# Optimization experiments

Measured on AMD Instinct MI355X. Metric: run time of the kernel, lower is better.

Reference implementation:

```python
import jax, jax.numpy as jnp
import numpy as np

D_MODEL = 2048
NUM_HEADS = 32
NUM_GROUPS = 8
HEAD_DIM = D_MODEL // NUM_HEADS  # 64
HPG = NUM_HEADS // NUM_GROUPS    # heads per group = 4
B, S = 2, 2048


def setup_inputs() -> dict:
    key = jax.random.key(0)
    ks = jax.random.split(key, 11)
    sd = 1.0 / np.sqrt(D_MODEL)
    kv_dim = HEAD_DIM * NUM_GROUPS
    return {
        "q": jax.random.normal(ks[0], (B, S, D_MODEL), jnp.float32),
        "k": jax.random.normal(ks[1], (B, S, D_MODEL), jnp.float32),
        "v": jax.random.normal(ks[2], (B, S, D_MODEL), jnp.float32),
        "Wq": jax.random.normal(ks[3], (D_MODEL, D_MODEL), jnp.float32) * sd,
        "bq": jnp.zeros((D_MODEL,), jnp.float32),
        "Wk": jax.random.normal(ks[4], (D_MODEL, kv_dim), jnp.float32) * sd,
        "bk": jnp.zeros((kv_dim,), jnp.float32),
        "Wv": jax.random.normal(ks[5], (D_MODEL, kv_dim), jnp.float32) * sd,
        "bv": jnp.zeros((kv_dim,), jnp.float32),
        "Wo": jax.random.normal(ks[6], (D_MODEL, D_MODEL), jnp.float32) * sd,
        "bo": jnp.zeros((D_MODEL,), jnp.float32),
    }


def reference(q, k, v, Wq, bq, Wk, bk, Wv, bv, Wo, bo):
    b, qlen, _ = q.shape
    kvlen = k.shape[1]
    # projections
    qh = (q @ Wq + bq).reshape(b, qlen, NUM_GROUPS, HPG, HEAD_DIM)   # [b,s,g,h,d]
    kh = (k @ Wk + bk).reshape(b, kvlen, NUM_GROUPS, HEAD_DIM)        # [b,t,g,d]
    vh = (v @ Wv + bv).reshape(b, kvlen, NUM_GROUPS, HEAD_DIM)        # [b,t,g,d]
    scale = 1.0 / np.sqrt(HEAD_DIM).astype(np.float32)
    # grouped attention: each group's heads share the same K/V
    scores = jnp.einsum('bsghd,btgd->bghst', qh, kh) * scale          # [b,g,h,s,t]
    attn = jax.nn.softmax(scores, axis=-1)                            # dropout = identity (eval)
    out = jnp.einsum('bghst,btgd->bsghd', attn, vh)                   # [b,s,g,h,d]
    out = out.reshape(b, qlen, D_MODEL)
    return out @ Wo + bo
```

## Files before the change

kernel.cpp:

```cpp
#include <hip/hip_runtime.h>

typedef unsigned short u16;
typedef unsigned int u32;
typedef __attribute__((ext_vector_type(8))) short bf16x8;
typedef __attribute__((ext_vector_type(4))) float f32x4;
typedef __attribute__((ext_vector_type(16))) float f32x16;

#define DM 2048
#define SQ_SCALE (0.125f * 1.44269504089f)

__device__ __forceinline__ u16 f2bf(float f) {
  union { float f; u32 u; } v; v.f = f;
  u32 r = v.u + 0x7fffu + ((v.u >> 16) & 1u);
  return (u16)(r >> 16);
}
__device__ __forceinline__ u32 pkrn(float lo, float hi) {
  union { float f; u32 u; } a, b; a.f = lo; b.f = hi;
  return ((a.u + 0x8000u) >> 16) | ((b.u + 0x8000u) & 0xffff0000u);
}
__device__ __forceinline__ void gload16(const u16* g, u16* l) {
  __builtin_amdgcn_global_load_lds((const __attribute__((address_space(1))) void*)g,
                                   (__attribute__((address_space(3))) void*)l, 16, 0, 0);
}

__global__ __launch_bounds__(256) void cast3(const float* __restrict__ a0,
                                             const float* __restrict__ a1,
                                             const float* __restrict__ a2,
                                             u16* __restrict__ o0,
                                             u16* __restrict__ o1,
                                             u16* __restrict__ o2) {
  const float* in; u16* out;
  if (blockIdx.z == 0) { in = a0; out = o0; }
  else if (blockIdx.z == 1) { in = a1; out = o1; }
  else { in = a2; out = o2; }
  size_t i = ((size_t)blockIdx.x * 256 + threadIdx.x) * 8;
  float4 f0 = *(const float4*)(in + i);
  float4 f1 = *(const float4*)(in + i + 4);
  uint4 w = {pkrn(f0.x, f0.y), pkrn(f0.z, f0.w), pkrn(f1.x, f1.y), pkrn(f1.z, f1.w)};
  *(uint4*)(out + i) = w;
}

__global__ __launch_bounds__(256) void transpose_cast(const float* __restrict__ in,
                                                      u16* __restrict__ out,
                                                      int K, int N) {
  __shared__ u16 s[64][72];
  int n0 = blockIdx.x * 64, k0 = blockIdx.y * 64;
  int t = threadIdx.x;
  int r = t >> 2;
  int cc = (t & 3) * 16;
  const float* ip = in + (size_t)(k0 + r) * N + n0 + cc;
  u16 tmp[16];
#pragma unroll
  for (int i = 0; i < 16; i += 4) {
    float4 v = *(const float4*)(ip + i);
    tmp[i] = f2bf(v.x); tmp[i + 1] = f2bf(v.y);
    tmp[i + 2] = f2bf(v.z); tmp[i + 3] = f2bf(v.w);
  }
  *(uint4*)&s[r][cc] = *(uint4*)tmp;
  *(uint4*)&s[r][cc + 8] = *(uint4*)(tmp + 8);
  __syncthreads();
#pragma unroll
  for (int i = 0; i < 16; i++) tmp[i] = s[cc + i][r];
  u16* op = out + (size_t)(n0 + r) * K + k0 + cc;
  *(uint4*)op = *(uint4*)tmp;
  *(uint4*)(op + 8) = *(uint4*)(tmp + 8);
}

__global__ __launch_bounds__(256) void transpose_v(const u16* __restrict__ kvb,
                                                   u16* __restrict__ vtb) {
  __shared__ u16 s[64][72];
  int bg = blockIdx.y;
  int t0 = blockIdx.x * 64;
  int t = threadIdx.x;
  int r = t >> 2;
  int cc = (t & 3) * 16;
  const u16* ip = kvb + ((size_t)(bg >> 3) * 2048 + t0 + r) * 1024 + 512 + (bg & 7) * 64 + cc;
  *(uint4*)&s[r][cc] = *(const uint4*)ip;
  *(uint4*)&s[r][cc + 8] = *(const uint4*)(ip + 8);
  __syncthreads();
  u16 tmp[16];
#pragma unroll
  for (int i = 0; i < 16; i++) tmp[i] = s[cc + i][r];
  u16* op = vtb + (size_t)bg * 64 * 2048 + (size_t)r * 2048 + t0 + cc;
  *(uint4*)op = *(uint4*)tmp;
  *(uint4*)(op + 8) = *(uint4*)(tmp + 8);
}

__global__ __launch_bounds__(256) void gemm_proj(const u16* __restrict__ qb,
                                                 const u16* __restrict__ kb,
                                                 const u16* __restrict__ vb,
                                                 const u16* __restrict__ Bt,
                                                 const float* __restrict__ bqp,
                                                 const float* __restrict__ bkp,
                                                 const float* __restrict__ bvp,
                                                 u16* __restrict__ qhb,
                                                 u16* __restrict__ kvb) {
  __shared__ u16 As[128 * 32];
  __shared__ u16 Bs[128 * 32];
  int n0 = blockIdx.x * 128, m0 = blockIdx.y * 128;
  const u16* A; const float* bias; u16* C; int cw, bofs; float esc;
  if (n0 < 2048)      { A = qb; bias = bqp; C = qhb; cw = 2048; bofs = 0;    esc = SQ_SCALE; }
  else if (n0 < 2560) { A = kb; bias = bkp; C = kvb; cw = 1024; bofs = 2048; esc = 1.0f; }
  else                { A = vb; bias = bvp; C = kvb; cw = 1024; bofs = 2560; esc = 1.0f; }
  int ccol0 = (n0 < 2048) ? n0 : (n0 - 2048);

  int tid = threadIdx.x, wave = tid >> 6, lane = tid & 63;
  int lq = lane & 15, quad = lane >> 4;
  int wm = (wave & 1) * 64, wn = (wave >> 1) * 64;

  f32x4 zero = {0.f, 0.f, 0.f, 0.f};
  f32x4 acc[4][4];
#pragma unroll
  for (int i = 0; i < 4; i++)
#pragma unroll
    for (int j = 0; j < 4; j++) acc[i][j] = zero;

  const u16* gA = A + (size_t)(m0 + wave * 16 + (lane >> 2)) * 2048 + (lane & 3) * 8;
  const u16* gB = Bt + (size_t)(n0 + wave * 16 + (lane >> 2)) * 2048 + (lane & 3) * 8;
  u16* lA0 = &As[(wave * 16) * 32];
  u16* lA1 = &As[(64 + wave * 16) * 32];
  u16* lB0 = &Bs[(wave * 16) * 32];
  u16* lB1 = &Bs[(64 + wave * 16) * 32];

  for (int k0 = 0; k0 < 2048; k0 += 32) {
    __syncthreads();
    gload16(gA + k0, lA0);
    gload16(gA + (size_t)64 * 2048 + k0, lA1);
    gload16(gB + k0, lB0);
    gload16(gB + (size_t)64 * 2048 + k0, lB1);
    __syncthreads();
    bf16x8 af[4], bf[4];
#pragma unroll
    for (int i = 0; i < 4; i++) af[i] = *(const bf16x8*)&As[(wm + i * 16 + lq) * 32 + quad * 8];
#pragma unroll
    for (int j = 0; j < 4; j++) bf[j] = *(const bf16x8*)&Bs[(wn + j * 16 + lq) * 32 + quad * 8];
#pragma unroll
    for (int i = 0; i < 4; i++)
#pragma unroll
      for (int j = 0; j < 4; j++)
        acc[i][j] = __builtin_amdgcn_mfma_f32_16x16x32_bf16(af[i], bf[j], acc[i][j], 0, 0, 0);
  }
#pragma unroll
  for (int j = 0; j < 4; j++) {
    int nglob = n0 + wn + j * 16 + lq;
    float bv = bias[nglob - bofs];
    int col = ccol0 + wn + j * 16 + lq;
#pragma unroll
    for (int i = 0; i < 4; i++) {
#pragma unroll
      for (int rg = 0; rg < 4; rg++) {
        int row = m0 + wm + i * 16 + quad * 4 + rg;
        C[(size_t)row * cw + col] = f2bf((acc[i][j][rg] + bv) * esc);
      }
    }
  }
}

__global__ __launch_bounds__(256) void gemm_o(const u16* __restrict__ A,
                                              const u16* __restrict__ Bt,
                                              const float* __restrict__ bias,
                                              float* __restrict__ C) {
  __shared__ u16 As[128 * 32];
  __shared__ u16 Bs[128 * 32];
  int n0 = blockIdx.x * 128, m0 = blockIdx.y * 128;
  int tid = threadIdx.x, wave = tid >> 6, lane = tid & 63;
  int lq = lane & 15, quad = lane >> 4;
  int wm = (wave & 1) * 64, wn = (wave >> 1) * 64;

  f32x4 zero = {0.f, 0.f, 0.f, 0.f};
  f32x4 acc[4][4];
#pragma unroll
  for (int i = 0; i < 4; i++)
#pragma unroll
    for (int j = 0; j < 4; j++) acc[i][j] = zero;

  const u16* gA = A + (size_t)(m0 + wave * 16 + (lane >> 2)) * 2048 + (lane & 3) * 8;
  const u16* gB = Bt + (size_t)(n0 + wave * 16 + (lane >> 2)) * 2048 + (lane & 3) * 8;
  u16* lA0 = &As[(wave * 16) * 32];
  u16* lA1 = &As[(64 + wave * 16) * 32];
  u16* lB0 = &Bs[(wave * 16) * 32];
  u16* lB1 = &Bs[(64 + wave * 16) * 32];

  for (int k0 = 0; k0 < 2048; k0 += 32) {
    __syncthreads();
    gload16(gA + k0, lA0);
    gload16(gA + (size_t)64 * 2048 + k0, lA1);
    gload16(gB + k0, lB0);
    gload16(gB + (size_t)64 * 2048 + k0, lB1);
    __syncthreads();
    bf16x8 af[4], bf[4];
#pragma unroll
    for (int i = 0; i < 4; i++) af[i] = *(const bf16x8*)&As[(wm + i * 16 + lq) * 32 + quad * 8];
#pragma unroll
    for (int j = 0; j < 4; j++) bf[j] = *(const bf16x8*)&Bs[(wn + j * 16 + lq) * 32 + quad * 8];
#pragma unroll
    for (int i = 0; i < 4; i++)
#pragma unroll
      for (int j = 0; j < 4; j++)
        acc[i][j] = __builtin_amdgcn_mfma_f32_16x16x32_bf16(af[i], bf[j], acc[i][j], 0, 0, 0);
  }
#pragma unroll
  for (int j = 0; j < 4; j++) {
    int col = n0 + wn + j * 16 + lq;
    float bv = bias[col];
#pragma unroll
    for (int i = 0; i < 4; i++) {
#pragma unroll
      for (int rg = 0; rg < 4; rg++) {
        int row = m0 + wm + i * 16 + quad * 4 + rg;
        C[(size_t)row * 2048 + col] = acc[i][j][rg] + bv;
      }
    }
  }
}

__global__ __launch_bounds__(256) void attn2(const u16* __restrict__ qh,
                                             const u16* __restrict__ kvb,
                                             const u16* __restrict__ vtb,
                                             u16* __restrict__ out) {
  __shared__ u16 Ks[32][72];
  __shared__ u16 Vs[64][40];
  __shared__ float Ls[4][2][32];
  int flat = blockIdx.x + (blockIdx.y << 3);
  int w = ((flat & 7) << 6) + (flat >> 3);
  int head = w >> 3;
  int b = head >> 5, g = (head >> 2) & 7, h = head & 3;
  int tid = threadIdx.x, wave = tid >> 6, lane = tid & 63;
  int lh = lane & 31, hi = lane >> 5;
  const int qoff = (g * 4 + h) * 64;
  const int koff = g * 64;
  int sBase = (w & 7) * 256 + wave * 64;

  bf16x8 qf[2][4];
#pragma unroll
  for (int sb = 0; sb < 2; sb++)
#pragma unroll
    for (int st = 0; st < 4; st++)
      qf[sb][st] = *(const bf16x8*)(qh + (size_t)(b * 2048 + sBase + sb * 32 + lh) * DM +
                                    qoff + st * 16 + hi * 8);

  f32x16 o_acc[2][2];
#pragma unroll
  for (int sb = 0; sb < 2; sb++)
#pragma unroll
    for (int db = 0; db < 2; db++)
#pragma unroll
      for (int r = 0; r < 16; r++) o_acc[sb][db][r] = 0.f;
  float l_acc[2] = {0.f, 0.f};

  int sr = tid >> 3, sc = (tid & 7) * 8;
  int vd = tid >> 2, vc = (tid & 3) * 8;
  const u16* kbase = kvb + (size_t)b * 2048 * 1024 + koff;
  const u16* vbase = vtb + (size_t)(head >> 2) * 64 * 2048 + (size_t)vd * 2048;

  uint4 kreg = *(const uint4*)(kbase + (size_t)sr * 1024 + sc);
  uint4 vreg = *(const uint4*)(vbase + vc);

  for (int t0 = 0; t0 < 2048; t0 += 32) {
    __syncthreads();
    *(uint4*)&Ks[sr][sc] = kreg;
    *(uint4*)&Vs[vd][vc] = vreg;
    __syncthreads();
    int tn = (t0 + 32 < 2048) ? t0 + 32 : 0;
    kreg = *(const uint4*)(kbase + (size_t)(tn + sr) * 1024 + sc);
    vreg = *(const uint4*)(vbase + tn + vc);

    bf16x8 kf[4], vf[2][2];
#pragma unroll
    for (int st = 0; st < 4; st++) kf[st] = *(const bf16x8*)&Ks[lh][st * 16 + hi * 8];
#pragma unroll
    for (int T = 0; T < 2; T++)
#pragma unroll
      for (int db = 0; db < 2; db++)
        vf[T][db] = *(const bf16x8*)&Vs[db * 32 + lh][T * 16 + hi * 8];

#pragma unroll
    for (int sb = 0; sb < 2; sb++) {
      f32x16 st_acc;
#pragma unroll
      for (int r = 0; r < 16; r++) st_acc[r] = 0.f;
      __builtin_amdgcn_s_setprio(1);
#pragma unroll
      for (int st = 0; st < 4; st++)
        st_acc = __builtin_amdgcn_mfma_f32_32x32x16_bf16(kf[st], qf[sb][st], st_acc, 0, 0, 0);
      __builtin_amdgcn_s_setprio(0);
      float pr[16];
#pragma unroll
      for (int r = 0; r < 16; r++) pr[r] = __builtin_amdgcn_exp2f(st_acc[r]);
      float s0 = ((pr[0] + pr[1]) + (pr[2] + pr[3])) + ((pr[4] + pr[5]) + (pr[6] + pr[7]));
      float s1 = ((pr[8] + pr[9]) + (pr[10] + pr[11])) + ((pr[12] + pr[13]) + (pr[14] + pr[15]));
      l_acc[sb] += s0 + s1;
      u32 pk[8];
#pragma unroll
      for (int a = 0; a < 4; a++) {
        pk[2 * a] = pkrn(pr[4 * a], pr[4 * a + 1]);
        pk[2 * a + 1] = pkrn(pr[4 * a + 2], pr[4 * a + 3]);
      }
#pragma unroll
      for (int T = 0; T < 2; T++) {
        u32 E0 = hi ? pk[4 * T] : pk[4 * T + 2];
        u32 E1 = hi ? pk[4 * T + 1] : pk[4 * T + 3];
        u32 X0 = __shfl_xor(E0, 32);
        u32 X1 = __shfl_xor(E1, 32);
        union { u32 u[4]; bf16x8 v; } af;
        af.u[0] = hi ? X0 : pk[4 * T];
        af.u[1] = hi ? X1 : pk[4 * T + 1];
        af.u[2] = hi ? pk[4 * T + 2] : X0;
        af.u[3] = hi ? pk[4 * T + 3] : X1;
        __builtin_amdgcn_s_setprio(1);
#pragma unroll
        for (int db = 0; db < 2; db++)
          o_acc[sb][db] = __builtin_amdgcn_mfma_f32_32x32x16_bf16(af.v, vf[T][db], o_acc[sb][db], 0, 0, 0);
        __builtin_amdgcn_s_setprio(0);
      }
    }
  }

#pragma unroll
  for (int sb = 0; sb < 2; sb++) {
    float lt = l_acc[sb] + __shfl_xor(l_acc[sb], 32);
    Ls[wave][sb][lh] = 1.0f / lt;
  }
  __builtin_amdgcn_wave_barrier();
#pragma unroll
  for (int sb = 0; sb < 2; sb++) {
    f32x4 inv[4];
#pragma unroll
    for (int a = 0; a < 4; a++) inv[a] = *(const f32x4*)&Ls[wave][sb][8 * a + 4 * hi];
#pragma unroll
    for (int db = 0; db < 2; db++) {
#pragma unroll
      for (int r = 0; r < 16; r++) {
        int srow = (r & 3) + 8 * (r >> 2) + 4 * hi;
        size_t o = (size_t)(b * 2048 + sBase + sb * 32 + srow) * DM + qoff + db * 32 + lh;
        out[o] = f2bf(o_acc[sb][db][r] * inv[r >> 2][r & 3]);
      }
    }
  }
}

extern "C" void kernel_launch(void* const* d_in, const int* in_sizes, int n_in,
                              void* d_out, int out_size, void* d_ws, size_t ws_size,
                              hipStream_t stream) {
  const float* q  = (const float*)d_in[0];
  const float* k  = (const float*)d_in[1];
  const float* v  = (const float*)d_in[2];
  const float* Wq = (const float*)d_in[3];
  const float* bq = (const float*)d_in[4];
  const float* Wk = (const float*)d_in[5];
  const float* bk = (const float*)d_in[6];
  const float* Wv = (const float*)d_in[7];
  const float* bv = (const float*)d_in[8];
  const float* Wo = (const float*)d_in[9];
  const float* bo = (const float*)d_in[10];

  u16* p = (u16*)d_ws;
  u16* WqkvT = p; p += (size_t)3072 * 2048;
  u16* WoT   = p; p += (size_t)2048 * 2048;
  u16* qb    = p; p += (size_t)4096 * 2048;
  u16* kb    = p; p += (size_t)4096 * 2048;
  u16* vb    = p; p += (size_t)4096 * 2048;
  u16* qhb   = p; p += (size_t)4096 * 2048;
  u16* kvb   = p; p += (size_t)4096 * 1024;
  u16* vtb   = p; p += (size_t)16 * 64 * 2048;
  u16* att   = qb;

  cast3<<<dim3(4096, 1, 3), 256, 0, stream>>>(q, k, v, qb, kb, vb);

  transpose_cast<<<dim3(32, 32), 256, 0, stream>>>(Wq, WqkvT, 2048, 2048);
  transpose_cast<<<dim3(8, 32), 256, 0, stream>>>(Wk, WqkvT + (size_t)2048 * 2048, 2048, 512);
  transpose_cast<<<dim3(8, 32), 256, 0, stream>>>(Wv, WqkvT + (size_t)2560 * 2048, 2048, 512);
  transpose_cast<<<dim3(32, 32), 256, 0, stream>>>(Wo, WoT, 2048, 2048);

  gemm_proj<<<dim3(24, 32), 256, 0, stream>>>(qb, kb, vb, WqkvT, bq, bk, bv, qhb, kvb);

  transpose_v<<<dim3(32, 16), 256, 0, stream>>>(kvb, vtb);

  attn2<<<dim3(8, 64), 256, 0, stream>>>(qhb, kvb, vtb, att);

  gemm_o<<<dim3(16, 32), 256, 0, stream>>>(att, WoT, bo, (float*)d_out);
}
```

Measured before the change: 414.5 us.

## Halve query rows per attention wave, double grid, use hardware bf16 pack

```diff
diff --git a/kernel.cpp b/kernel.cpp
--- a/kernel.cpp
+++ b/kernel.cpp
@@ -17,6 +17,11 @@
 __device__ __forceinline__ u32 pkrn(float lo, float hi) {
   union { float f; u32 u; } a, b; a.f = lo; b.f = hi;
   return ((a.u + 0x8000u) >> 16) | ((b.u + 0x8000u) & 0xffff0000u);
+}
+__device__ __forceinline__ u32 cvtpk(float lo, float hi) {
+  u32 r;
+  asm("v_cvt_pk_bf16_f32 %0, %1, %2" : "=v"(r) : "v"(lo), "v"(hi));
+  return r;
 }
 __device__ __forceinline__ void gload16(const u16* g, u16* l) {
   __builtin_amdgcn_global_load_lds((const __attribute__((address_space(1))) void*)g,
@@ -220,33 +225,29 @@
                                              u16* __restrict__ out) {
   __shared__ u16 Ks[32][72];
   __shared__ u16 Vs[64][40];
-  __shared__ float Ls[4][2][32];
-  int flat = blockIdx.x + (blockIdx.y << 3);
-  int w = ((flat & 7) << 6) + (flat >> 3);
-  int head = w >> 3;
+  __shared__ float Ls[4][32];
+  int flat = blockIdx.x + (blockIdx.y << 4);
+  int w = ((flat & 7) << 7) + (flat >> 3);
+  int head = w >> 4;
   int b = head >> 5, g = (head >> 2) & 7, h = head & 3;
   int tid = threadIdx.x, wave = tid >> 6, lane = tid & 63;
   int lh = lane & 31, hi = lane >> 5;
   const int qoff = (g * 4 + h) * 64;
   const int koff = g * 64;
-  int sBase = (w & 7) * 256 + wave * 64;
-
-  bf16x8 qf[2][4];
-#pragma unroll
-  for (int sb = 0; sb < 2; sb++)
-#pragma unroll
-    for (int st = 0; st < 4; st++)
-      qf[sb][st] = *(const bf16x8*)(qh + (size_t)(b * 2048 + sBase + sb * 32 + lh) * DM +
-                                    qoff + st * 16 + hi * 8);
-
-  f32x16 o_acc[2][2];
-#pragma unroll
-  for (int sb = 0; sb < 2; sb++)
-#pragma unroll
-    for (int db = 0; db < 2; db++)
-#pragma unroll
-      for (int r = 0; r < 16; r++) o_acc[sb][db][r] = 0.f;
-  float l_acc[2] = {0.f, 0.f};
+  int sBase = (w & 15) * 128 + wave * 32;
+
+  bf16x8 qf[4];
+#pragma unroll
+  for (int st = 0; st < 4; st++)
+    qf[st] = *(const bf16x8*)(qh + (size_t)(b * 2048 + sBase + lh) * DM +
+                              qoff + st * 16 + hi * 8);
+
+  f32x16 o_acc[2];
+#pragma unroll
+  for (int db = 0; db < 2; db++)
+#pragma unroll
+    for (int r = 0; r < 16; r++) o_acc[db][r] = 0.f;
+  float l_acc = 0.f;
 
   int sr = tid >> 3, sc = (tid & 7) * 8;
   int vd = tid >> 2, vc = (tid & 3) * 8;
@@ -274,66 +275,61 @@
       for (int db = 0; db < 2; db++)
         vf[T][db] = *(const bf16x8*)&Vs[db * 32 + lh][T * 16 + hi * 8];
 
-#pragma unroll
-    for (int sb = 0; sb < 2; sb++) {
-      f32x16 st_acc;
-#pragma unroll
-      for (int r = 0; r < 16; r++) st_acc[r] = 0.f;
+    f32x16 st_acc;
+#pragma unroll
+    for (int r = 0; r < 16; r++) st_acc[r] = 0.f;
+    __builtin_amdgcn_s_setprio(1);
+#pragma unroll
+    for (int st = 0; st < 4; st++)
+      st_acc = __builtin_amdgcn_mfma_f32_32x32x16_bf16(kf[st], qf[st], st_acc, 0, 0, 0);
+    __builtin_amdgcn_s_setprio(0);
+    float pr[16];
+#pragma unroll
+    for (int r = 0; r < 16; r++) pr[r] = __builtin_amdgcn_exp2f(st_acc[r]);
+    float s0 = ((pr[0] + pr[1]) + (pr[2] + pr[3])) + ((pr[4] + pr[5]) + (pr[6] + pr[7]));
+    float s1 = ((pr[8] + pr[9]) + (pr[10] + pr[11])) + ((pr[12] + pr[13]) + (pr[14] + pr[15]));
+    l_acc += s0 + s1;
+    u32 pk[8];
+#pragma unroll
+    for (int a = 0; a < 4; a++) {
+      pk[2 * a] = cvtpk(pr[4 * a], pr[4 * a + 1]);
+      pk[2 * a + 1] = cvtpk(pr[4 * a + 2], pr[4 * a + 3]);
+    }
+#pragma unroll
+    for (int T = 0; T < 2; T++) {
+      u32 E0 = hi ? pk[4 * T] : pk[4 * T + 2];
+      u32 E1 = hi ? pk[4 * T + 1] : pk[4 * T + 3];
+      u32 X0 = __shfl_xor(E0, 32);
+      u32 X1 = __shfl_xor(E1, 32);
+      union { u32 u[4]; bf16x8 v; } af;
+      af.u[0] = hi ? X0 : pk[4 * T];
+      af.u[1] = hi ? X1 : pk[4 * T + 1];
+      af.u[2] = hi ? pk[4 * T + 2] : X0;
+      af.u[3] = hi ? pk[4 * T + 3] : X1;
       __builtin_amdgcn_s_setprio(1);
 #pragma unroll
-      for (int st = 0; st < 4; st++)
-        st_acc = __builtin_amdgcn_mfma_f32_32x32x16_bf16(kf[st], qf[sb][st], st_acc, 0, 0, 0);
+      for (int db = 0; db < 2; db++)
+        o_acc[db] = __builtin_amdgcn_mfma_f32_32x32x16_bf16(af.v, vf[T][db], o_acc[db], 0, 0, 0);
       __builtin_amdgcn_s_setprio(0);
-      float pr[16];
-#pragma unroll
-      for (int r = 0; r < 16; r++) pr[r] = __builtin_amdgcn_exp2f(st_acc[r]);
-      float s0 = ((pr[0] + pr[1]) + (pr[2] + pr[3])) + ((pr[4] + pr[5]) + (pr[6] + pr[7]));
-      float s1 = ((pr[8] + pr[9]) + (pr[10] + pr[11])) + ((pr[12] + pr[13]) + (pr[14] + pr[15]));
-      l_acc[sb] += s0 + s1;
-      u32 pk[8];
-#pragma unroll
-      for (int a = 0; a < 4; a++) {
-        pk[2 * a] = pkrn(pr[4 * a], pr[4 * a + 1]);
-        pk[2 * a + 1] = pkrn(pr[4 * a + 2], pr[4 * a + 3]);
-      }
-#pragma unroll
-      for (int T = 0; T < 2; T++) {
-        u32 E0 = hi ? pk[4 * T] : pk[4 * T + 2];
-        u32 E1 = hi ? pk[4 * T + 1] : pk[4 * T + 3];
-        u32 X0 = __shfl_xor(E0, 32);
-        u32 X1 = __shfl_xor(E1, 32);
-        union { u32 u[4]; bf16x8 v; } af;
-        af.u[0] = hi ? X0 : pk[4 * T];
-        af.u[1] = hi ? X1 : pk[4 * T + 1];
-        af.u[2] = hi ? pk[4 * T + 2] : X0;
-        af.u[3] = hi ? pk[4 * T + 3] : X1;
-        __builtin_amdgcn_s_setprio(1);
-#pragma unroll
-        for (int db = 0; db < 2; db++)
-          o_acc[sb][db] = __builtin_amdgcn_mfma_f32_32x32x16_bf16(af.v, vf[T][db], o_acc[sb][db], 0, 0, 0);
-        __builtin_amdgcn_s_setprio(0);
-      }
-    }
-  }
-
-#pragma unroll
-  for (int sb = 0; sb < 2; sb++) {
-    float lt = l_acc[sb] + __shfl_xor(l_acc[sb], 32);
-    Ls[wave][sb][lh] = 1.0f / lt;
+    }
+  }
+
+  {
+    float lt = l_acc + __shfl_xor(l_acc, 32);
+    Ls[wave][lh] = 1.0f / lt;
   }
   __builtin_amdgcn_wave_barrier();
-#pragma unroll
-  for (int sb = 0; sb < 2; sb++) {
+  {
     f32x4 inv[4];
 #pragma unroll
-    for (int a = 0; a < 4; a++) inv[a] = *(const f32x4*)&Ls[wave][sb][8 * a + 4 * hi];
+    for (int a = 0; a < 4; a++) inv[a] = *(const f32x4*)&Ls[wave][8 * a + 4 * hi];
 #pragma unroll
     for (int db = 0; db < 2; db++) {
 #pragma unroll
       for (int r = 0; r < 16; r++) {
         int srow = (r & 3) + 8 * (r >> 2) + 4 * hi;
-        size_t o = (size_t)(b * 2048 + sBase + sb * 32 + srow) * DM + qoff + db * 32 + lh;
-        out[o] = f2bf(o_acc[sb][db][r] * inv[r >> 2][r & 3]);
+        size_t o = (size_t)(b * 2048 + sBase + srow) * DM + qoff + db * 32 + lh;
+        out[o] = f2bf(o_acc[db][r] * inv[r >> 2][r & 3]);
       }
     }
   }
@@ -376,7 +372,7 @@
 
   transpose_v<<<dim3(32, 16), 256, 0, stream>>>(kvb, vtb);
 
-  attn2<<<dim3(8, 64), 256, 0, stream>>>(qhb, kvb, vtb, att);
+  attn2<<<dim3(16, 64), 256, 0, stream>>>(qhb, kvb, vtb, att);
 
   gemm_o<<<dim3(16, 32), 256, 0, stream>>>(att, WoT, bo, (float*)d_out);
 }
```

Result: no change. 411.5 us (-0.7%).
